# Optimization experiments

Hardware: AMD Instinct MI355X
Metric: run time of the kernel (lower is better)

The kernel has to match this reference:

```python
import jax, jax.numpy as jnp
import numpy as np

BINS = 8

def setup_inputs() -> dict:
    key = jax.random.key(0)
    k1, k2, k3 = jax.random.split(key, 3)
    B, H, W = 32, 160, 160
    HW = H * W
    reg_logits = jax.random.normal(k1, (B, 4 * BINS, H, W), dtype=jnp.float32)
    targets = jax.random.uniform(k2, (B, HW, 4), dtype=jnp.float32) * (BINS - 1)
    pos_mask = jax.random.randint(k3, (B, HW), 0, 2) == 1
    return {"reg_logits": reg_logits, "targets": targets, "pos_mask": pos_mask}

def reference(reg_logits, targets, pos_mask):
    bins = BINS
    B, C, H, W = reg_logits.shape
    HW = H * W
    # [B, C, H, W] -> [B, HW, 4, bins]
    rl = reg_logits.transpose(0, 2, 3, 1).reshape(B, HW, 4, bins)
    t = jnp.clip(targets, 0.0, bins - 1 - 0.0001)          # [B, HW, 4]
    l_id = jnp.floor(t).astype(jnp.int32)
    u_id = jnp.minimum(l_id + 1, bins - 1)
    w_u = t - l_id.astype(t.dtype)
    w_l = 1.0 - w_u
    logp = jax.nn.log_softmax(rl, axis=-1)                 # [B, HW, 4, bins]
    nll_l = -jnp.take_along_axis(logp, l_id[..., None], axis=-1)[..., 0]
    nll_u = -jnp.take_along_axis(logp, u_id[..., None], axis=-1)[..., 0]
    per = w_l * nll_l + w_u * nll_u                        # [B, HW, 4]
    m = pos_mask.astype(per.dtype)                         # [B, HW]
    npos = jnp.sum(m)
    # mean over positives per coordinate, averaged over 4 coords ==
    # sum over (positives x 4) / (npos * 4)
    total = jnp.sum(per * m[..., None])
    loss = total / (jnp.maximum(npos, 1.0) * 4.0)
    return jnp.where(npos > 0, loss, jnp.zeros((), dtype=per.dtype))
```

## Files before the change

### kernel.cpp

```cpp
#include <hip/hip_runtime.h>

#define BINS 8
#define BLOCK 256
#define NB 768

constexpr int BATCH   = 32;
constexpr int HW      = 25600;
constexpr int NGROUPS = BATCH * HW / 4;

__global__ void init_acc_kernel(float* acc) {
    acc[0] = 0.0f;
    acc[1] = 0.0f;
    ((unsigned*)acc)[2] = 0u;
}

__device__ __forceinline__ float comp4(const float4& v, int i) {
    return (i == 0) ? v.x : (i == 1) ? v.y : (i == 2) ? v.z : v.w;
}

__global__ __launch_bounds__(BLOCK) void dfl_main_kernel(
    const float* __restrict__ logits,
    const float* __restrict__ targets,
    const int*   __restrict__ mask,
    float* __restrict__ acc,
    float* __restrict__ out) {

    float tsum = 0.0f;
    float tcnt = 0.0f;

    for (int g = blockIdx.x * BLOCK + threadIdx.x; g < NGROUPS; g += NB * BLOCK) {
        const int p4 = g << 2;
        const int b  = p4 / HW;
        const int pp = p4 - b * HW;

        const float* base = logits + (size_t)b * 4 * BINS * HW + pp;

        const float4* tgt = (const float4*)(targets + (size_t)p4 * 4);
        float4 t4[4];
#pragma unroll
        for (int i = 0; i < 4; ++i) t4[i] = tgt[i];

        const int4 mk = *(const int4*)(mask + p4);
        float msk[4];
        msk[0] = mk.x ? 1.0f : 0.0f;
        msk[1] = mk.y ? 1.0f : 0.0f;
        msk[2] = mk.z ? 1.0f : 0.0f;
        msk[3] = mk.w ? 1.0f : 0.0f;
        tcnt += msk[0] + msk[1] + msk[2] + msk[3];

#pragma unroll
        for (int c = 0; c < 4; ++c) {
            float4 xv[BINS];
#pragma unroll
            for (int j = 0; j < BINS; ++j)
                xv[j] = *(const float4*)(base + (size_t)(c * BINS + j) * HW);

#pragma unroll
            for (int i = 0; i < 4; ++i) {
                float x[BINS];
#pragma unroll
                for (int j = 0; j < BINS; ++j) x[j] = comp4(xv[j], i);

                float t = comp4(t4[i], c);
                t = fminf(fmaxf(t, 0.0f), (float)(BINS - 1) - 0.0001f);
                float lf = floorf(t);
                int   li = (int)lf;
                int   ui = li + 1;
                float wu = t - lf;
                float wl = 1.0f - wu;

                float s = 0.0f;
#pragma unroll
                for (int j = 0; j < BINS; ++j) s += __expf(x[j]);
                float lse = __logf(s);

                float xl = x[0], xu = x[0];
#pragma unroll
                for (int j = 1; j < BINS; ++j) {
                    xl = (li == j) ? x[j] : xl;
                    xu = (ui == j) ? x[j] : xu;
                }

                tsum += msk[i] * (lse - (wl * xl + wu * xu));
            }
        }
    }

#pragma unroll
    for (int off = 32; off > 0; off >>= 1) {
        tsum += __shfl_down(tsum, off, 64);
        tcnt += __shfl_down(tcnt, off, 64);
    }

    __shared__ float ssum[BLOCK / 64];
    __shared__ float scnt[BLOCK / 64];
    const int wid  = threadIdx.x >> 6;
    const int lane = threadIdx.x & 63;
    if (lane == 0) { ssum[wid] = tsum; scnt[wid] = tcnt; }
    __syncthreads();

    if (threadIdx.x == 0) {
        float bs = 0.0f, bc = 0.0f;
#pragma unroll
        for (int w = 0; w < BLOCK / 64; ++w) { bs += ssum[w]; bc += scnt[w]; }
        atomicAdd(&acc[0], bs);
        atomicAdd(&acc[1], bc);
        __threadfence();
        unsigned done = atomicAdd((unsigned*)acc + 2, 1u);
        if (done == NB - 1) {
            float total = atomicAdd(&acc[0], 0.0f);
            float npos  = atomicAdd(&acc[1], 0.0f);
            float loss  = total / (fmaxf(npos, 1.0f) * 4.0f);
            out[0] = (npos > 0.0f) ? loss : 0.0f;
        }
    }
}

extern "C" void kernel_launch(void* const* d_in, const int* in_sizes, int n_in,
                              void* d_out, int out_size, void* d_ws, size_t ws_size,
                              hipStream_t stream) {
    const float* logits  = (const float*)d_in[0];
    const float* targets = (const float*)d_in[1];
    const int*   mask    = (const int*)d_in[2];
    float* out = (float*)d_out;
    float* acc = (float*)d_ws;

    init_acc_kernel<<<1, 1, 0, stream>>>(acc);
    dfl_main_kernel<<<NB, BLOCK, 0, stream>>>(logits, targets, mask, acc, out);
}
```

Before: 203.8 us.

## Use one-shot grid with two pixels per thread and separate finalize kernel

Replaces the persistent grid-stride loop (768 blocks, 4 pixels per thread, float4 loads) with a grid that covers all pixels once, each thread handling 2 pixels with float2 loads. The last-block completion counter and threadfence are replaced by a separate finalize kernel launch. The goal is more memory-level parallelism and occupancy (launch bounds hint of 6 blocks), at the cost of narrower loads, many more blocks issuing atomics on the same two addresses, and an extra kernel launch.

Measured after the change: 186.6 us. -8.4%, faster.

```diff
diff --git a/kernel.cpp b/kernel.cpp
--- a/kernel.cpp
+++ b/kernel.cpp
@@ -2,87 +2,77 @@
 
 #define BINS 8
 #define BLOCK 256
-#define NB 768
 
-constexpr int BATCH   = 32;
-constexpr int HW      = 25600;
-constexpr int NGROUPS = BATCH * HW / 4;
+constexpr int BATCH    = 32;
+constexpr int HW       = 25600;
+constexpr int NPIX     = BATCH * HW;
+constexpr int NTHREADS = NPIX / 2;
+constexpr int NBLOCKS  = NTHREADS / BLOCK;
 
 __global__ void init_acc_kernel(float* acc) {
     acc[0] = 0.0f;
     acc[1] = 0.0f;
-    ((unsigned*)acc)[2] = 0u;
 }
 
-__device__ __forceinline__ float comp4(const float4& v, int i) {
-    return (i == 0) ? v.x : (i == 1) ? v.y : (i == 2) ? v.z : v.w;
-}
-
-__global__ __launch_bounds__(BLOCK) void dfl_main_kernel(
+__global__ __launch_bounds__(BLOCK, 6) void dfl_main_kernel(
     const float* __restrict__ logits,
     const float* __restrict__ targets,
     const int*   __restrict__ mask,
-    float* __restrict__ acc,
-    float* __restrict__ out) {
+    float* __restrict__ acc) {
+
+    const int g  = blockIdx.x * BLOCK + threadIdx.x;
+    const int p2 = g << 1;
+    const int b  = p2 / HW;
+    const int pp = p2 - b * HW;
+
+    const float* base = logits + (size_t)b * 4 * BINS * HW + pp;
+
+    const float4* tgt = (const float4*)(targets + (size_t)p2 * 4);
+    const float4 t0 = tgt[0];
+    const float4 t1 = tgt[1];
+
+    const int2 mk = *(const int2*)(mask + p2);
+    const float m0 = mk.x ? 1.0f : 0.0f;
+    const float m1 = mk.y ? 1.0f : 0.0f;
 
     float tsum = 0.0f;
-    float tcnt = 0.0f;
-
-    for (int g = blockIdx.x * BLOCK + threadIdx.x; g < NGROUPS; g += NB * BLOCK) {
-        const int p4 = g << 2;
-        const int b  = p4 / HW;
-        const int pp = p4 - b * HW;
-
-        const float* base = logits + (size_t)b * 4 * BINS * HW + pp;
-
-        const float4* tgt = (const float4*)(targets + (size_t)p4 * 4);
-        float4 t4[4];
-#pragma unroll
-        for (int i = 0; i < 4; ++i) t4[i] = tgt[i];
-
-        const int4 mk = *(const int4*)(mask + p4);
-        float msk[4];
-        msk[0] = mk.x ? 1.0f : 0.0f;
-        msk[1] = mk.y ? 1.0f : 0.0f;
-        msk[2] = mk.z ? 1.0f : 0.0f;
-        msk[3] = mk.w ? 1.0f : 0.0f;
-        tcnt += msk[0] + msk[1] + msk[2] + msk[3];
+    float tcnt = m0 + m1;
 
 #pragma unroll
-        for (int c = 0; c < 4; ++c) {
-            float4 xv[BINS];
+    for (int c = 0; c < 4; ++c) {
+        float2 xv[BINS];
 #pragma unroll
-            for (int j = 0; j < BINS; ++j)
-                xv[j] = *(const float4*)(base + (size_t)(c * BINS + j) * HW);
+        for (int j = 0; j < BINS; ++j)
+            xv[j] = *(const float2*)(base + (size_t)(c * BINS + j) * HW);
 
 #pragma unroll
-            for (int i = 0; i < 4; ++i) {
-                float x[BINS];
+        for (int i = 0; i < 2; ++i) {
+            float x[BINS];
 #pragma unroll
-                for (int j = 0; j < BINS; ++j) x[j] = comp4(xv[j], i);
+            for (int j = 0; j < BINS; ++j) x[j] = i ? xv[j].y : xv[j].x;
 
-                float t = comp4(t4[i], c);
-                t = fminf(fmaxf(t, 0.0f), (float)(BINS - 1) - 0.0001f);
-                float lf = floorf(t);
-                int   li = (int)lf;
-                int   ui = li + 1;
-                float wu = t - lf;
-                float wl = 1.0f - wu;
+            const float4& tv = i ? t1 : t0;
+            float t = (c == 0) ? tv.x : (c == 1) ? tv.y : (c == 2) ? tv.z : tv.w;
+            t = fminf(fmaxf(t, 0.0f), (float)(BINS - 1) - 0.0001f);
+            float lf = floorf(t);
+            int   li = (int)lf;
+            int   ui = li + 1;
+            float wu = t - lf;
+            float wl = 1.0f - wu;
 
-                float s = 0.0f;
+            float s = 0.0f;
 #pragma unroll
-                for (int j = 0; j < BINS; ++j) s += __expf(x[j]);
-                float lse = __logf(s);
+            for (int j = 0; j < BINS; ++j) s += __expf(x[j]);
+            float lse = __logf(s);
 
-                float xl = x[0], xu = x[0];
+            float xl = x[0], xu = x[0];
 #pragma unroll
-                for (int j = 1; j < BINS; ++j) {
-                    xl = (li == j) ? x[j] : xl;
-                    xu = (ui == j) ? x[j] : xu;
-                }
+            for (int j = 1; j < BINS; ++j) {
+                xl = (li == j) ? x[j] : xl;
+                xu = (ui == j) ? x[j] : xu;
+            }
 
-                tsum += msk[i] * (lse - (wl * xl + wu * xu));
-            }
+            tsum += (i ? m1 : m0) * (lse - (wl * xl + wu * xu));
         }
     }
 
@@ -98,22 +88,21 @@
     const int lane = threadIdx.x & 63;
     if (lane == 0) { ssum[wid] = tsum; scnt[wid] = tcnt; }
     __syncthreads();
-
     if (threadIdx.x == 0) {
         float bs = 0.0f, bc = 0.0f;
 #pragma unroll
         for (int w = 0; w < BLOCK / 64; ++w) { bs += ssum[w]; bc += scnt[w]; }
         atomicAdd(&acc[0], bs);
         atomicAdd(&acc[1], bc);
-        __threadfence();
-        unsigned done = atomicAdd((unsigned*)acc + 2, 1u);
-        if (done == NB - 1) {
-            float total = atomicAdd(&acc[0], 0.0f);
-            float npos  = atomicAdd(&acc[1], 0.0f);
-            float loss  = total / (fmaxf(npos, 1.0f) * 4.0f);
-            out[0] = (npos > 0.0f) ? loss : 0.0f;
-        }
     }
+}
+
+__global__ void finalize_kernel(const float* __restrict__ acc,
+                                float* __restrict__ out) {
+    float total = acc[0];
+    float npos  = acc[1];
+    float loss  = total / (fmaxf(npos, 1.0f) * 4.0f);
+    out[0] = (npos > 0.0f) ? loss : 0.0f;
 }
 
 extern "C" void kernel_launch(void* const* d_in, const int* in_sizes, int n_in,
@@ -126,5 +115,6 @@
     float* acc = (float*)d_ws;
 
     init_acc_kernel<<<1, 1, 0, stream>>>(acc);
-    dfl_main_kernel<<<NB, BLOCK, 0, stream>>>(logits, targets, mask, acc, out);
+    dfl_main_kernel<<<NBLOCKS, BLOCK, 0, stream>>>(logits, targets, mask, acc);
+    finalize_kernel<<<1, 1, 0, stream>>>(acc, out);
 }
```

## Replace grid-stride loop with one group per thread and per-wave atomics

Applied to the files above, without the earlier changes.

Drops the persistent grid-stride loop and launches one thread per 4-pixel group (1600 blocks of 128), so many more waves are in flight to hide memory latency. The block-level shared-memory reduction and last-block completion counter are replaced by per-wavefront atomics plus a separate finalize kernel. This adds an extra kernel launch and many more global atomics (two per wave) in exchange for removing the loop and the block synchronisation.

Result: slower. 234.3 us (+15.0%).

```diff
diff --git a/kernel.cpp b/kernel.cpp
--- a/kernel.cpp
+++ b/kernel.cpp
@@ -1,17 +1,17 @@
 #include <hip/hip_runtime.h>
 
 #define BINS 8
-#define BLOCK 256
-#define NB 768
+#define BLOCK 128
 
 constexpr int BATCH   = 32;
 constexpr int HW      = 25600;
-constexpr int NGROUPS = BATCH * HW / 4;
+constexpr int NPIX    = BATCH * HW;
+constexpr int NGROUPS = NPIX / 4;
+constexpr int NBLOCKS = NGROUPS / BLOCK;
 
 __global__ void init_acc_kernel(float* acc) {
     acc[0] = 0.0f;
     acc[1] = 0.0f;
-    ((unsigned*)acc)[2] = 0u;
 }
 
 __device__ __forceinline__ float comp4(const float4& v, int i) {
@@ -22,67 +22,64 @@
     const float* __restrict__ logits,
     const float* __restrict__ targets,
     const int*   __restrict__ mask,
-    float* __restrict__ acc,
-    float* __restrict__ out) {
+    float* __restrict__ acc) {
+
+    const int g  = blockIdx.x * BLOCK + threadIdx.x;
+    const int p4 = g << 2;
+    const int b  = p4 / HW;
+    const int pp = p4 - b * HW;
+
+    const float* base = logits + (size_t)b * 4 * BINS * HW + pp;
+
+    const float4* tgt = (const float4*)(targets + (size_t)p4 * 4);
+    float4 t4[4];
+#pragma unroll
+    for (int i = 0; i < 4; ++i) t4[i] = tgt[i];
+
+    const int4 mk = *(const int4*)(mask + p4);
+    float msk[4];
+    msk[0] = mk.x ? 1.0f : 0.0f;
+    msk[1] = mk.y ? 1.0f : 0.0f;
+    msk[2] = mk.z ? 1.0f : 0.0f;
+    msk[3] = mk.w ? 1.0f : 0.0f;
 
     float tsum = 0.0f;
-    float tcnt = 0.0f;
-
-    for (int g = blockIdx.x * BLOCK + threadIdx.x; g < NGROUPS; g += NB * BLOCK) {
-        const int p4 = g << 2;
-        const int b  = p4 / HW;
-        const int pp = p4 - b * HW;
-
-        const float* base = logits + (size_t)b * 4 * BINS * HW + pp;
-
-        const float4* tgt = (const float4*)(targets + (size_t)p4 * 4);
-        float4 t4[4];
-#pragma unroll
-        for (int i = 0; i < 4; ++i) t4[i] = tgt[i];
-
-        const int4 mk = *(const int4*)(mask + p4);
-        float msk[4];
-        msk[0] = mk.x ? 1.0f : 0.0f;
-        msk[1] = mk.y ? 1.0f : 0.0f;
-        msk[2] = mk.z ? 1.0f : 0.0f;
-        msk[3] = mk.w ? 1.0f : 0.0f;
-        tcnt += msk[0] + msk[1] + msk[2] + msk[3];
+    float tcnt = msk[0] + msk[1] + msk[2] + msk[3];
 
 #pragma unroll
-        for (int c = 0; c < 4; ++c) {
-            float4 xv[BINS];
+    for (int c = 0; c < 4; ++c) {
+        float4 xv[BINS];
 #pragma unroll
-            for (int j = 0; j < BINS; ++j)
-                xv[j] = *(const float4*)(base + (size_t)(c * BINS + j) * HW);
+        for (int j = 0; j < BINS; ++j)
+            xv[j] = *(const float4*)(base + (size_t)(c * BINS + j) * HW);
 
 #pragma unroll
-            for (int i = 0; i < 4; ++i) {
-                float x[BINS];
+        for (int i = 0; i < 4; ++i) {
+            float x[BINS];
 #pragma unroll
-                for (int j = 0; j < BINS; ++j) x[j] = comp4(xv[j], i);
+            for (int j = 0; j < BINS; ++j) x[j] = comp4(xv[j], i);
 
-                float t = comp4(t4[i], c);
-                t = fminf(fmaxf(t, 0.0f), (float)(BINS - 1) - 0.0001f);
-                float lf = floorf(t);
-                int   li = (int)lf;
-                int   ui = li + 1;
-                float wu = t - lf;
-                float wl = 1.0f - wu;
+            float t = comp4(t4[i], c);
+            t = fminf(fmaxf(t, 0.0f), (float)(BINS - 1) - 0.0001f);
+            float lf = floorf(t);
+            int   li = (int)lf;
+            int   ui = li + 1;
+            float wu = t - lf;
+            float wl = 1.0f - wu;
 
-                float s = 0.0f;
+            float s = 0.0f;
 #pragma unroll
-                for (int j = 0; j < BINS; ++j) s += __expf(x[j]);
-                float lse = __logf(s);
+            for (int j = 0; j < BINS; ++j) s += __expf(x[j]);
+            float lse = __logf(s);
 
-                float xl = x[0], xu = x[0];
+            float xl = x[0], xu = x[0];
 #pragma unroll
-                for (int j = 1; j < BINS; ++j) {
-                    xl = (li == j) ? x[j] : xl;
-                    xu = (ui == j) ? x[j] : xu;
-                }
+            for (int j = 1; j < BINS; ++j) {
+                xl = (li == j) ? x[j] : xl;
+                xu = (ui == j) ? x[j] : xu;
+            }
 
-                tsum += msk[i] * (lse - (wl * xl + wu * xu));
-            }
+            tsum += msk[i] * (lse - (wl * xl + wu * xu));
         }
     }
 
@@ -91,29 +88,18 @@
         tsum += __shfl_down(tsum, off, 64);
         tcnt += __shfl_down(tcnt, off, 64);
     }
+    if ((threadIdx.x & 63) == 0) {
+        atomicAdd(&acc[0], tsum);
+        atomicAdd(&acc[1], tcnt);
+    }
+}
 
-    __shared__ float ssum[BLOCK / 64];
-    __shared__ float scnt[BLOCK / 64];
-    const int wid  = threadIdx.x >> 6;
-    const int lane = threadIdx.x & 63;
-    if (lane == 0) { ssum[wid] = tsum; scnt[wid] = tcnt; }
-    __syncthreads();
-
-    if (threadIdx.x == 0) {
-        float bs = 0.0f, bc = 0.0f;
-#pragma unroll
-        for (int w = 0; w < BLOCK / 64; ++w) { bs += ssum[w]; bc += scnt[w]; }
-        atomicAdd(&acc[0], bs);
-        atomicAdd(&acc[1], bc);
-        __threadfence();
-        unsigned done = atomicAdd((unsigned*)acc + 2, 1u);
-        if (done == NB - 1) {
-            float total = atomicAdd(&acc[0], 0.0f);
-            float npos  = atomicAdd(&acc[1], 0.0f);
-            float loss  = total / (fmaxf(npos, 1.0f) * 4.0f);
-            out[0] = (npos > 0.0f) ? loss : 0.0f;
-        }
-    }
+__global__ void finalize_kernel(const float* __restrict__ acc,
+                                float* __restrict__ out) {
+    float total = acc[0];
+    float npos  = acc[1];
+    float loss  = total / (fmaxf(npos, 1.0f) * 4.0f);
+    out[0] = (npos > 0.0f) ? loss : 0.0f;
 }
 
 extern "C" void kernel_launch(void* const* d_in, const int* in_sizes, int n_in,
@@ -126,5 +112,6 @@
     float* acc = (float*)d_ws;
 
     init_acc_kernel<<<1, 1, 0, stream>>>(acc);
-    dfl_main_kernel<<<NB, BLOCK, 0, stream>>>(logits, targets, mask, acc, out);
+    dfl_main_kernel<<<NBLOCKS, BLOCK, 0, stream>>>(logits, targets, mask, acc);
+    finalize_kernel<<<1, 1, 0, stream>>>(acc, out);
 }
```

## Replace grid-stride atomics with one-group-per-thread and a separate finalize reduction kernel

Applied to the files above, without the earlier changes.

Launches one thread per 4-pixel group instead of a fixed 768-block grid-stride loop. Each block writes its partial sum and count to the workspace instead of updating global atomics, and a single-block finalize kernel reduces them and computes the loss. This removes the init kernel, the atomics and the last-block fence logic, at the cost of an extra dependent launch and a slightly uneven final wave of blocks.

Result: faster. 171.6 us (-15.8%).

```diff
diff --git a/kernel.cpp b/kernel.cpp
--- a/kernel.cpp
+++ b/kernel.cpp
@@ -2,17 +2,12 @@
 
 #define BINS 8
 #define BLOCK 256
-#define NB 768
 
 constexpr int BATCH   = 32;
 constexpr int HW      = 25600;
-constexpr int NGROUPS = BATCH * HW / 4;
-
-__global__ void init_acc_kernel(float* acc) {
-    acc[0] = 0.0f;
-    acc[1] = 0.0f;
-    ((unsigned*)acc)[2] = 0u;
-}
+constexpr int NPIX    = BATCH * HW;
+constexpr int NGROUPS = NPIX / 4;
+constexpr int NBLOCKS = NGROUPS / BLOCK;
 
 __device__ __forceinline__ float comp4(const float4& v, int i) {
     return (i == 0) ? v.x : (i == 1) ? v.y : (i == 2) ? v.z : v.w;
@@ -22,67 +17,64 @@
     const float* __restrict__ logits,
     const float* __restrict__ targets,
     const int*   __restrict__ mask,
-    float* __restrict__ acc,
-    float* __restrict__ out) {
+    float* __restrict__ partials) {
+
+    const int g  = blockIdx.x * BLOCK + threadIdx.x;
+    const int p4 = g << 2;
+    const int b  = p4 / HW;
+    const int pp = p4 - b * HW;
+
+    const float* base = logits + (size_t)b * 4 * BINS * HW + pp;
+
+    const float4* tgt = (const float4*)(targets + (size_t)p4 * 4);
+    float4 t4[4];
+#pragma unroll
+    for (int i = 0; i < 4; ++i) t4[i] = tgt[i];
+
+    const int4 mk = *(const int4*)(mask + p4);
+    float msk[4];
+    msk[0] = mk.x ? 1.0f : 0.0f;
+    msk[1] = mk.y ? 1.0f : 0.0f;
+    msk[2] = mk.z ? 1.0f : 0.0f;
+    msk[3] = mk.w ? 1.0f : 0.0f;
 
     float tsum = 0.0f;
-    float tcnt = 0.0f;
-
-    for (int g = blockIdx.x * BLOCK + threadIdx.x; g < NGROUPS; g += NB * BLOCK) {
-        const int p4 = g << 2;
-        const int b  = p4 / HW;
-        const int pp = p4 - b * HW;
-
-        const float* base = logits + (size_t)b * 4 * BINS * HW + pp;
-
-        const float4* tgt = (const float4*)(targets + (size_t)p4 * 4);
-        float4 t4[4];
-#pragma unroll
-        for (int i = 0; i < 4; ++i) t4[i] = tgt[i];
-
-        const int4 mk = *(const int4*)(mask + p4);
-        float msk[4];
-        msk[0] = mk.x ? 1.0f : 0.0f;
-        msk[1] = mk.y ? 1.0f : 0.0f;
-        msk[2] = mk.z ? 1.0f : 0.0f;
-        msk[3] = mk.w ? 1.0f : 0.0f;
-        tcnt += msk[0] + msk[1] + msk[2] + msk[3];
+    float tcnt = msk[0] + msk[1] + msk[2] + msk[3];
 
 #pragma unroll
-        for (int c = 0; c < 4; ++c) {
-            float4 xv[BINS];
+    for (int c = 0; c < 4; ++c) {
+        float4 xv[BINS];
 #pragma unroll
-            for (int j = 0; j < BINS; ++j)
-                xv[j] = *(const float4*)(base + (size_t)(c * BINS + j) * HW);
+        for (int j = 0; j < BINS; ++j)
+            xv[j] = *(const float4*)(base + (size_t)(c * BINS + j) * HW);
 
 #pragma unroll
-            for (int i = 0; i < 4; ++i) {
-                float x[BINS];
+        for (int i = 0; i < 4; ++i) {
+            float x[BINS];
 #pragma unroll
-                for (int j = 0; j < BINS; ++j) x[j] = comp4(xv[j], i);
+            for (int j = 0; j < BINS; ++j) x[j] = comp4(xv[j], i);
 
-                float t = comp4(t4[i], c);
-                t = fminf(fmaxf(t, 0.0f), (float)(BINS - 1) - 0.0001f);
-                float lf = floorf(t);
-                int   li = (int)lf;
-                int   ui = li + 1;
-                float wu = t - lf;
-                float wl = 1.0f - wu;
+            float t = comp4(t4[i], c);
+            t = fminf(fmaxf(t, 0.0f), (float)(BINS - 1) - 0.0001f);
+            float lf = floorf(t);
+            int   li = (int)lf;
+            int   ui = li + 1;
+            float wu = t - lf;
+            float wl = 1.0f - wu;
 
-                float s = 0.0f;
+            float s = 0.0f;
 #pragma unroll
-                for (int j = 0; j < BINS; ++j) s += __expf(x[j]);
-                float lse = __logf(s);
+            for (int j = 0; j < BINS; ++j) s += __expf(x[j]);
+            float lse = __logf(s);
 
-                float xl = x[0], xu = x[0];
+            float xl = x[0], xu = x[0];
 #pragma unroll
-                for (int j = 1; j < BINS; ++j) {
-                    xl = (li == j) ? x[j] : xl;
-                    xu = (ui == j) ? x[j] : xu;
-                }
+            for (int j = 1; j < BINS; ++j) {
+                xl = (li == j) ? x[j] : xl;
+                xu = (ui == j) ? x[j] : xu;
+            }
 
-                tsum += msk[i] * (lse - (wl * xl + wu * xu));
-            }
+            tsum += msk[i] * (lse - (wl * xl + wu * xu));
         }
     }
 
@@ -98,21 +90,40 @@
     const int lane = threadIdx.x & 63;
     if (lane == 0) { ssum[wid] = tsum; scnt[wid] = tcnt; }
     __syncthreads();
-
     if (threadIdx.x == 0) {
         float bs = 0.0f, bc = 0.0f;
 #pragma unroll
         for (int w = 0; w < BLOCK / 64; ++w) { bs += ssum[w]; bc += scnt[w]; }
-        atomicAdd(&acc[0], bs);
-        atomicAdd(&acc[1], bc);
-        __threadfence();
-        unsigned done = atomicAdd((unsigned*)acc + 2, 1u);
-        if (done == NB - 1) {
-            float total = atomicAdd(&acc[0], 0.0f);
-            float npos  = atomicAdd(&acc[1], 0.0f);
-            float loss  = total / (fmaxf(npos, 1.0f) * 4.0f);
-            out[0] = (npos > 0.0f) ? loss : 0.0f;
-        }
+        partials[2 * blockIdx.x]     = bs;
+        partials[2 * blockIdx.x + 1] = bc;
+    }
+}
+
+__global__ __launch_bounds__(BLOCK) void finalize_kernel(
+    const float* __restrict__ partials, float* __restrict__ out) {
+
+    float tsum = 0.0f, tcnt = 0.0f;
+    for (int i = threadIdx.x; i < NBLOCKS; i += BLOCK) {
+        tsum += partials[2 * i];
+        tcnt += partials[2 * i + 1];
+    }
+#pragma unroll
+    for (int off = 32; off > 0; off >>= 1) {
+        tsum += __shfl_down(tsum, off, 64);
+        tcnt += __shfl_down(tcnt, off, 64);
+    }
+    __shared__ float ssum[BLOCK / 64];
+    __shared__ float scnt[BLOCK / 64];
+    const int wid  = threadIdx.x >> 6;
+    const int lane = threadIdx.x & 63;
+    if (lane == 0) { ssum[wid] = tsum; scnt[wid] = tcnt; }
+    __syncthreads();
+    if (threadIdx.x == 0) {
+        float total = 0.0f, npos = 0.0f;
+#pragma unroll
+        for (int w = 0; w < BLOCK / 64; ++w) { total += ssum[w]; npos += scnt[w]; }
+        float loss = total / (fmaxf(npos, 1.0f) * 4.0f);
+        out[0] = (npos > 0.0f) ? loss : 0.0f;
     }
 }
 
@@ -122,9 +133,9 @@
     const float* logits  = (const float*)d_in[0];
     const float* targets = (const float*)d_in[1];
     const int*   mask    = (const int*)d_in[2];
-    float* out = (float*)d_out;
-    float* acc = (float*)d_ws;
+    float* out      = (float*)d_out;
+    float* partials = (float*)d_ws;
 
-    init_acc_kernel<<<1, 1, 0, stream>>>(acc);
-    dfl_main_kernel<<<NB, BLOCK, 0, stream>>>(logits, targets, mask, acc, out);
+    dfl_main_kernel<<<NBLOCKS, BLOCK, 0, stream>>>(logits, targets, mask, partials);
+    finalize_kernel<<<1, BLOCK, 0, stream>>>(partials, out);
 }
```
